# Kernel tuning notes

Hardware: AMD Instinct MI355X
Metric: run time of the kernel (lower is better)

Reference implementation:

```python
import jax, jax.numpy as jnp
import numpy as np

DIM = 256
NEG_SLOPE = 0.01  # torch F.leaky_relu default


def setup_inputs() -> dict:
    key = jax.random.key(0)
    ks = jax.random.split(key, 10)
    B, O, I, D = 16, 64, 512, DIM
    q = jax.random.normal(ks[0], (B, O, D), dtype=jnp.float32)
    k = jax.random.normal(ks[1], (B, I, D), dtype=jnp.float32)
    v = jax.random.normal(ks[2], (B, I, D), dtype=jnp.float32)
    mask = jax.random.randint(ks[3], (B, I), 0, 2).astype(bool)  # 1/True = pad
    s = 1.0 / np.sqrt(2 * D)
    # score MLP: Linear(2D -> D), tanh, Linear(D -> 1)
    W1 = jax.random.normal(ks[4], (D, 2 * D), dtype=jnp.float32) * s
    b1 = jnp.zeros((D,), dtype=jnp.float32)
    W2 = jax.random.normal(ks[5], (1, D), dtype=jnp.float32) * (1.0 / np.sqrt(D))
    b2 = jnp.zeros((1,), dtype=jnp.float32)
    # output projection fw: Linear(D -> D)
    Wf = jax.random.normal(ks[6], (D, D), dtype=jnp.float32) * (1.0 / np.sqrt(D))
    bf = jnp.zeros((D,), dtype=jnp.float32)
    return {"q": q, "k": k, "v": v, "mask": mask,
            "W1": W1, "b1": b1, "W2": W2, "b2": b2, "Wf": Wf, "bf": bf}


def reference(q, k, v, mask, W1, b1, W2, b2, Wf, bf):
    # Linear over concat([q, k]) decomposes exactly: W1 @ [q;k] = W1q@q + W1k@k
    D = q.shape[-1]
    W1q, W1k = W1[:, :D], W1[:, D:]
    qp = jnp.einsum('bod,hd->boh', q, W1q)          # (B, O, D)
    kp = jnp.einsum('bid,hd->bih', k, W1k)          # (B, I, D)
    h = jnp.tanh(qp[:, :, None, :] + kp[:, None, :, :] + b1)  # (B, O, I, D)
    score = jnp.einsum('boih,h->boi', h, W2[0]) + b2[0]       # (B, O, I)
    score = jnp.where(mask[:, None, :], -jnp.inf, score)
    attn = jax.nn.softmax(score, axis=-1)           # (B, O, I)
    out = jnp.einsum('boi,bid->bod', attn, v)       # (B, O, D)
    out = out @ Wf.T + bf                           # dropout in eval mode = identity
    out = jnp.where(out >= 0, out, NEG_SLOPE * out) # leaky_relu
    return out, attn
```

## Files before the change

kernel.cpp:

```cpp
#include <hip/hip_runtime.h>
#include <math.h>

#define DIM 256
#define BATCH 16
#define NO 64
#define NI 512
#define NEG_SLOPE 0.01f
#define CSCALE 2.885390081777927f
#define OT 2

typedef float f32x4 __attribute__((ext_vector_type(4)));
typedef __bf16 bf16x8 __attribute__((ext_vector_type(8)));
typedef unsigned int u32x4 __attribute__((ext_vector_type(4)));

__global__ __launch_bounds__(512) void mask_scan_kernel(
    const int* __restrict__ mask, int* __restrict__ idx,
    int* __restrict__ posArr, int* __restrict__ cnt)
{
  __shared__ int wtot[8];
  __shared__ int woff[8];
  const int b = blockIdx.x, t = threadIdx.x;
  const int lane = t & 63, wid = t >> 6;
  const int unm = (mask[b * NI + t] == 0) ? 1 : 0;
  unsigned long long bal = __ballot(unm);
  int my  = __popcll(bal & ((1ull << lane) - 1ull));
  if (lane == 0) wtot[wid] = __popcll(bal);
  __syncthreads();
  if (t == 0) {
    int acc = 0;
    for (int w = 0; w < 8; ++w) { woff[w] = acc; acc += wtot[w]; }
    cnt[b] = acc;
  }
  __syncthreads();
  int pos = woff[wid] + my;
  if (unm) idx[b * NI + pos] = t;
  posArr[b * NI + t] = unm ? pos : -1;
}

__device__ __forceinline__ void split2(float f, unsigned int& hi16, float& lo) {
  unsigned int u = __builtin_bit_cast(unsigned int, f);
  unsigned int h = (u + 0x7FFFu + ((u >> 16) & 1u)) & 0xFFFF0000u;
  hi16 = h >> 16;
  lo = f - __builtin_bit_cast(float, h);
}
__device__ __forceinline__ unsigned int rne16(float f) {
  unsigned int u = __builtin_bit_cast(unsigned int, f);
  return (u + 0x7FFFu + ((u >> 16) & 1u)) >> 16;
}

struct __align__(8) U2 { unsigned int x, y; };

#define OFF_AH 0
#define OFF_AL 9216
#define OFF_WH 18432
#define OFF_WL 27648

__global__ __launch_bounds__(256, 4) void proj_kernel(
    const float* __restrict__ q, const float* __restrict__ k,
    const float* __restrict__ W1, const float* __restrict__ b1,
    const float* __restrict__ Wf, const int* __restrict__ posArr,
    float* __restrict__ Eq, float* __restrict__ Ek4, float* __restrict__ WfT)
{
  __shared__ __align__(16) char smemRaw[36864];

  const int t  = threadIdx.x;
  const int bx = blockIdx.x;

  if (bx >= 576) {
    float* smem = (float*)smemRaw;
    const int tt = bx - 576;
    const int tr = tt >> 2, tc = tt & 3;
#pragma unroll
    for (int p = 0; p < 4; ++p) {
      int idx2 = p * 256 + t;
      int row = idx2 >> 4, j = idx2 & 15;
      float4 vv = *(const float4*)(Wf + (size_t)(tr * 64 + row) * 256 + tc * 64 + j * 4);
      *(float4*)&smem[row * 68 + j * 4] = vv;
    }
    __syncthreads();
#pragma unroll
    for (int p = 0; p < 4; ++p) {
      int idx2 = p * 256 + t;
      int row = idx2 >> 4, j = idx2 & 15;
      float4 ov;
      ov.x = smem[(j * 4 + 0) * 68 + row];
      ov.y = smem[(j * 4 + 1) * 68 + row];
      ov.z = smem[(j * 4 + 2) * 68 + row];
      ov.w = smem[(j * 4 + 3) * 68 + row];
      *(float4*)(WfT + (size_t)(tc * 64 + row) * 256 + tr * 64 + j * 4) = ov;
    }
    return;
  }

  const int mt = bx >> 2;
  const int nt = bx & 3;
  const int r0 = mt * 64;
  const int h0 = nt * 64;
  const bool isq = (r0 < BATCH * NO);
  const float* src = isq ? (q + (size_t)r0 * DIM)
                         : (k + (size_t)(r0 - BATCH * NO) * DIM);
  const int coff = isq ? 0 : DIM;

  const int srow = t >> 4;
  const int sc4  = t & 15;

  const int lane = t & 63, w = t >> 6;
  const int m0w = (w >> 1) * 32, n0w = (w & 1) * 32;
  const int lr = lane & 15, lg = lane >> 4;

  f32x4 acc[2][2] = {};

  float4 aR[4], wR[4];
#define LOADC(c0_)                                                              \
  _Pragma("unroll")                                                             \
  for (int p = 0; p < 4; ++p) {                                                 \
    int row = srow + p * 16;                                                    \
    aR[p] = *(const float4*)(src + (size_t)row * DIM + (c0_) + sc4 * 4);        \
    wR[p] = *(const float4*)(W1 + (size_t)(h0 + row) * (2 * DIM) + coff + (c0_) + sc4 * 4); \
  }

  LOADC(0)

  for (int c = 0; c < 4; ++c) {
#pragma unroll
    for (int p = 0; p < 4; ++p) {
      int row = srow + p * 16;
      int boff = row * 144 + sc4 * 8;
      unsigned int h0_, h1_, h2_, h3_;
      float l0, l1, l2, l3;
      split2(aR[p].x, h0_, l0); split2(aR[p].y, h1_, l1);
      split2(aR[p].z, h2_, l2); split2(aR[p].w, h3_, l3);
      *(U2*)(smemRaw + OFF_AH + boff) = { h0_ | (h1_ << 16), h2_ | (h3_ << 16) };
      *(U2*)(smemRaw + OFF_AL + boff) = { rne16(l0) | (rne16(l1) << 16),
                                          rne16(l2) | (rne16(l3) << 16) };
      split2(wR[p].x, h0_, l0); split2(wR[p].y, h1_, l1);
      split2(wR[p].z, h2_, l2); split2(wR[p].w, h3_, l3);
      *(U2*)(smemRaw + OFF_WH + boff) = { h0_ | (h1_ << 16), h2_ | (h3_ << 16) };
      *(U2*)(smemRaw + OFF_WL + boff) = { rne16(l0) | (rne16(l1) << 16),
                                          rne16(l2) | (rne16(l3) << 16) };
    }
    __syncthreads();

    if (c < 3) { LOADC((c + 1) * 64) }

#pragma unroll
    for (int kk = 0; kk < 2; ++kk) {
      const int kb = kk * 64 + lg * 16;
      bf16x8 ah[2], al[2], bh[2], bl[2];
#pragma unroll
      for (int mi = 0; mi < 2; ++mi) {
        int row = m0w + mi * 16 + lr;
        ah[mi] = __builtin_bit_cast(bf16x8, *(const u32x4*)(smemRaw + OFF_AH + row * 144 + kb));
        al[mi] = __builtin_bit_cast(bf16x8, *(const u32x4*)(smemRaw + OFF_AL + row * 144 + kb));
      }
#pragma unroll
      for (int ni = 0; ni < 2; ++ni) {
        int row = n0w + ni * 16 + lr;
        bh[ni] = __builtin_bit_cast(bf16x8, *(const u32x4*)(smemRaw + OFF_WH + row * 144 + kb));
        bl[ni] = __builtin_bit_cast(bf16x8, *(const u32x4*)(smemRaw + OFF_WL + row * 144 + kb));
      }
#pragma unroll
      for (int mi = 0; mi < 2; ++mi)
#pragma unroll
        for (int ni = 0; ni < 2; ++ni) {
          acc[mi][ni] = __builtin_amdgcn_mfma_f32_16x16x32_bf16(ah[mi], bh[ni], acc[mi][ni], 0, 0, 0);
          acc[mi][ni] = __builtin_amdgcn_mfma_f32_16x16x32_bf16(ah[mi], bl[ni], acc[mi][ni], 0, 0, 0);
          acc[mi][ni] = __builtin_amdgcn_mfma_f32_16x16x32_bf16(al[mi], bh[ni], acc[mi][ni], 0, 0, 0);
        }
    }
    __syncthreads();
  }

  if (isq) {
#pragma unroll
    for (int ni = 0; ni < 2; ++ni) {
      int h = h0 + n0w + ni * 16 + lr;
      float b1v = b1[h];
#pragma unroll
      for (int mi = 0; mi < 2; ++mi)
#pragma unroll
        for (int rg = 0; rg < 4; ++rg) {
          int r = r0 + m0w + mi * 16 + lg * 4 + rg;
          Eq[(size_t)r * DIM + h] =
              __builtin_amdgcn_exp2f((acc[mi][ni][rg] + b1v) * CSCALE);
        }
    }
  } else {
    const int rk0 = r0 - BATCH * NO;
    const int b = rk0 >> 9;
    const int ib = rk0 & 511;
#pragma unroll
    for (int mi = 0; mi < 2; ++mi)
#pragma unroll
      for (int rg = 0; rg < 4; ++rg) {
        int i = ib + m0w + mi * 16 + lg * 4 + rg;
        int pos = posArr[b * NI + i];
        if (pos >= 0) {
#pragma unroll
          for (int ni = 0; ni < 2; ++ni) {
            int h = h0 + n0w + ni * 16 + lr;
            Ek4[((size_t)(b * 64 + (h >> 2)) * NI + pos) * 4 + (h & 3)] =
                __builtin_amdgcn_exp2f(acc[mi][ni][rg] * CSCALE);
          }
        }
      }
  }
}

__device__ __forceinline__ void f4arr(float4 v, float* a) {
  a[0] = v.x; a[1] = v.y; a[2] = v.z; a[3] = v.w;
}

__global__ __launch_bounds__(512, 4) void attn_kernel(
    const float* __restrict__ Eq, const float* __restrict__ Ek4,
    const float* __restrict__ v, const int* __restrict__ idx,
    const int* __restrict__ posArr, const int* __restrict__ cnt,
    const float* __restrict__ W2, const float* __restrict__ b2,
    const float* __restrict__ WfT, const float* __restrict__ bf,
    float* __restrict__ out, float* __restrict__ attn_out)
{
  __shared__ float sc[OT][NI];
  __shared__ int   idxs[NI];
  __shared__ float pvp[8][OT][DIM];
  __shared__ float o0[OT][DIM];
  __shared__ float red4[8][OT];
  __shared__ float redw[8];

  const int t    = threadIdx.x;
  const int lane = t & 63;
  const int wid  = t >> 6;

  const int blk  = blockIdx.x;
  const int tile = (blk & 7) * 64 + (blk >> 3);
  const int b    = tile >> 5;
  const int bo0  = b * 64 + (tile & 31) * OT;

  const int cntb = cnt[b];
  idxs[t] = idx[b * NI + t];
  const int myPos = posArr[b * NI + t];

  float partial = (t < DIM) ? W2[t] : 0.f;
#pragma unroll
  for (int off = 32; off >= 1; off >>= 1) partial += __shfl_xor(partial, off, 64);
  if (lane == 0) redw[wid] = partial;
  __syncthreads();
  float sumw2 = 0.f;
#pragma unroll
  for (int w = 0; w < 8; ++w) sumw2 += redw[w];
  const float base = sumw2 + b2[0];

  const int j = t;
  const bool active = (j < cntb);
  const int jc = active ? j : (cntb > 0 ? cntb - 1 : 0);
  const float4* kb4 = (const float4*)Ek4 + (size_t)b * 64 * NI;
  const float* qrow0 = Eq + (size_t)(bo0 + 0) * DIM;
  const float* qrow1 = Eq + (size_t)(bo0 + 1) * DIM;

  float acc0 = 0.f, acc1 = 0.f;
  if (wid * 64 < cntb) {
#pragma unroll 8
    for (int hq = 0; hq < 64; ++hq) {
      float4 kq = kb4[(size_t)hq * NI + jc];
      float wr[4], q0r[4], q1r[4], kv[4];
      f4arr(*(const float4*)(W2 + hq * 4), wr);
      f4arr(*(const float4*)(qrow0 + hq * 4), q0r);
      f4arr(*(const float4*)(qrow1 + hq * 4), q1r);
      f4arr(kq, kv);
#pragma unroll
      for (int pr = 0; pr < 2; ++pr) {
        const int ea = pr * 2, eb = pr * 2 + 1;
        float A0 = fmaf(q0r[ea], kv[ea], 1.f);
        float B0 = fmaf(q0r[eb], kv[eb], 1.f);
        float N0 = fmaf(wr[eb], A0, wr[ea] * B0);
        acc0 = fmaf(N0, __builtin_amdgcn_rcpf(A0 * B0), acc0);
        float A1 = fmaf(q1r[ea], kv[ea], 1.f);
        float B1 = fmaf(q1r[eb], kv[eb], 1.f);
        float N1 = fmaf(wr[eb], A1, wr[ea] * B1);
        acc1 = fmaf(N1, __builtin_amdgcn_rcpf(A1 * B1), acc1);
      }
    }
  }

  float s0 = active ? (base - 2.f * acc0) : -INFINITY;
  float s1 = active ? (base - 2.f * acc1) : -INFINITY;

  float p0 = __builtin_amdgcn_exp2f(s0 * 1.4426950408889634f);
  float p1 = __builtin_amdgcn_exp2f(s1 * 1.4426950408889634f);
  float ps0 = p0, ps1 = p1;
#pragma unroll
  for (int off = 32; off >= 1; off >>= 1) {
    ps0 += __shfl_xor(ps0, off, 64);
    ps1 += __shfl_xor(ps1, off, 64);
  }
  __syncthreads();
  if (lane == 0) { red4[wid][0] = ps0; red4[wid][1] = ps1; }
  __syncthreads();
  float ss0 = 0.f, ss1 = 0.f;
#pragma unroll
  for (int w = 0; w < 8; ++w) { ss0 += red4[w][0]; ss1 += red4[w][1]; }
  const float a0 = p0 * __builtin_amdgcn_rcpf(ss0);
  const float a1 = p1 * __builtin_amdgcn_rcpf(ss1);
  sc[0][j] = a0;
  sc[1][j] = a1;
  __syncthreads();

  {
    float w0 = (myPos >= 0) ? sc[0][myPos] : 0.f;
    float w1 = (myPos >= 0) ? sc[1][myPos] : 0.f;
    attn_out[(size_t)(bo0 + 0) * NI + t] = w0;
    attn_out[(size_t)(bo0 + 1) * NI + t] = w1;
  }

  {
    const int d4 = lane;
    float4 av0 = {0.f, 0.f, 0.f, 0.f};
    float4 av1 = {0.f, 0.f, 0.f, 0.f};
    const float4* vb4 = (const float4*)(v + (size_t)b * NI * DIM);
    const int jend = min(wid * 64 + 64, cntb);
#pragma unroll 4
    for (int jb = wid * 64; jb < jend; ++jb) {
      int row = idxs[jb];
      float sa0 = sc[0][jb], sa1 = sc[1][jb];
      float4 vv = vb4[(size_t)row * 64 + d4];
      av0.x = fmaf(sa0, vv.x, av0.x);
      av0.y = fmaf(sa0, vv.y, av0.y);
      av0.z = fmaf(sa0, vv.z, av0.z);
      av0.w = fmaf(sa0, vv.w, av0.w);
      av1.x = fmaf(sa1, vv.x, av1.x);
      av1.y = fmaf(sa1, vv.y, av1.y);
      av1.z = fmaf(sa1, vv.z, av1.z);
      av1.w = fmaf(sa1, vv.w, av1.w);
    }
    *(float4*)&pvp[wid][0][d4 * 4] = av0;
    *(float4*)&pvp[wid][1][d4 * 4] = av1;
  }
  __syncthreads();
  {
    int oo = t >> 8, d = t & 255;
    float sacc = 0.f;
#pragma unroll
    for (int w = 0; w < 8; ++w) sacc += pvp[w][oo][d];
    o0[oo][d] = sacc;
  }
  __syncthreads();

  if (t < DIM) {
    const int d = t;
    float f0 = 0.f, f1 = 0.f;
#pragma unroll 8
    for (int e4 = 0; e4 < 64; ++e4) {
      float oa[4], ob[4];
      f4arr(*(const float4*)&o0[0][e4 * 4], oa);
      f4arr(*(const float4*)&o0[1][e4 * 4], ob);
#pragma unroll
      for (int c = 0; c < 4; ++c) {
        float wv = WfT[(size_t)(e4 * 4 + c) * DIM + d];
        f0 = fmaf(oa[c], wv, f0);
        f1 = fmaf(ob[c], wv, f1);
      }
    }
    float bfv = bf[d];
    f0 += bfv; f1 += bfv;
    f0 = (f0 >= 0.f) ? f0 : NEG_SLOPE * f0;
    f1 = (f1 >= 0.f) ? f1 : NEG_SLOPE * f1;
    out[(size_t)(bo0 + 0) * DIM + d] = f0;
    out[(size_t)(bo0 + 1) * DIM + d] = f1;
  }
}

extern "C" void kernel_launch(void* const* d_in, const int* in_sizes, int n_in,
                              void* d_out, int out_size, void* d_ws, size_t ws_size,
                              hipStream_t stream) {
  const float* q    = (const float*)d_in[0];
  const float* k    = (const float*)d_in[1];
  const float* v    = (const float*)d_in[2];
  const int*   mask = (const int*)d_in[3];
  const float* W1   = (const float*)d_in[4];
  const float* b1   = (const float*)d_in[5];
  const float* W2   = (const float*)d_in[6];
  const float* b2   = (const float*)d_in[7];
  const float* Wf   = (const float*)d_in[8];
  const float* bf   = (const float*)d_in[9];

  float* out      = (float*)d_out;
  float* attn_out = out + (size_t)BATCH * NO * DIM;

  float* Eq   = (float*)d_ws;
  float* Ek4  = Eq + (size_t)BATCH * NO * DIM;
  float* WfT  = Ek4 + (size_t)BATCH * DIM * NI;
  int*   idx  = (int*)(WfT + (size_t)DIM * DIM);
  int*   pos  = idx + BATCH * NI;
  int*   cnt  = pos + BATCH * NI;

  mask_scan_kernel<<<BATCH, 512, 0, stream>>>(mask, idx, pos, cnt);
  proj_kernel<<<592, 256, 0, stream>>>(q, k, W1, b1, Wf, pos, Eq, Ek4, WfT);
  attn_kernel<<<(BATCH * NO) / OT, 512, 0, stream>>>(Eq, Ek4, v, idx, pos, cnt,
                                                     W2, b2, WfT, bf, out, attn_out);
}
```

Measured before the change: 124.2 us.

## Fuse mask scan into projection and attention kernels, project only unmasked keys

Removes the separate mask_scan kernel launch. Each key-projection block now recomputes the per-batch prefix scan over the mask, gathers only unmasked key rows into its tile, and exits early when the tile lies beyond the unmasked count. This skips projection work for padded keys, which is about half of them with the test mask. The attention kernel recomputes the compacted index and positions from the mask with ballots. The cost is redundant scans in every block and gathered row loads.

```diff
diff --git a/kernel.cpp b/kernel.cpp
--- a/kernel.cpp
+++ b/kernel.cpp
@@ -13,30 +13,6 @@
 typedef __bf16 bf16x8 __attribute__((ext_vector_type(8)));
 typedef unsigned int u32x4 __attribute__((ext_vector_type(4)));
 
-__global__ __launch_bounds__(512) void mask_scan_kernel(
-    const int* __restrict__ mask, int* __restrict__ idx,
-    int* __restrict__ posArr, int* __restrict__ cnt)
-{
-  __shared__ int wtot[8];
-  __shared__ int woff[8];
-  const int b = blockIdx.x, t = threadIdx.x;
-  const int lane = t & 63, wid = t >> 6;
-  const int unm = (mask[b * NI + t] == 0) ? 1 : 0;
-  unsigned long long bal = __ballot(unm);
-  int my  = __popcll(bal & ((1ull << lane) - 1ull));
-  if (lane == 0) wtot[wid] = __popcll(bal);
-  __syncthreads();
-  if (t == 0) {
-    int acc = 0;
-    for (int w = 0; w < 8; ++w) { woff[w] = acc; acc += wtot[w]; }
-    cnt[b] = acc;
-  }
-  __syncthreads();
-  int pos = woff[wid] + my;
-  if (unm) idx[b * NI + pos] = t;
-  posArr[b * NI + t] = unm ? pos : -1;
-}
-
 __device__ __forceinline__ void split2(float f, unsigned int& hi16, float& lo) {
   unsigned int u = __builtin_bit_cast(unsigned int, f);
   unsigned int h = (u + 0x7FFFu + ((u >> 16) & 1u)) & 0xFFFF0000u;
@@ -58,10 +34,12 @@
 __global__ __launch_bounds__(256, 4) void proj_kernel(
     const float* __restrict__ q, const float* __restrict__ k,
     const float* __restrict__ W1, const float* __restrict__ b1,
-    const float* __restrict__ Wf, const int* __restrict__ posArr,
+    const float* __restrict__ Wf, const int* __restrict__ mask,
     float* __restrict__ Eq, float* __restrict__ Ek4, float* __restrict__ WfT)
 {
   __shared__ __align__(16) char smemRaw[36864];
+  __shared__ int idx_s[64];
+  __shared__ int swtot[4];
 
   const int t  = threadIdx.x;
   const int bx = blockIdx.x;
@@ -94,19 +72,58 @@
 
   const int mt = bx >> 2;
   const int nt = bx & 3;
-  const int r0 = mt * 64;
   const int h0 = nt * 64;
-  const bool isq = (r0 < BATCH * NO);
-  const float* src = isq ? (q + (size_t)r0 * DIM)
-                         : (k + (size_t)(r0 - BATCH * NO) * DIM);
-  const int coff = isq ? 0 : DIM;
+  const bool isq = (mt < 16);
 
   const int srow = t >> 4;
   const int sc4  = t & 15;
-
   const int lane = t & 63, w = t >> 6;
   const int m0w = (w >> 1) * 32, n0w = (w & 1) * 32;
   const int lr = lane & 15, lg = lane >> 4;
+
+  const float* src;
+  int coff, bb = 0, jb0 = 0, cntb = 0;
+  int rowg[4];
+
+  if (isq) {
+    src  = q + (size_t)(mt * 64) * DIM;
+    coff = 0;
+#pragma unroll
+    for (int p = 0; p < 4; ++p) rowg[p] = srow + p * 16;
+  } else {
+    const int ki = mt - 16;
+    bb  = ki >> 3;
+    jb0 = (ki & 7) * 64;
+    const int e0 = (mask[bb * NI + 2 * t] == 0);
+    const int e1 = (mask[bb * NI + 2 * t + 1] == 0);
+    const int ps = e0 + e1;
+    int x = ps;
+#pragma unroll
+    for (int off = 1; off < 64; off <<= 1) {
+      int y = __shfl_up(x, off, 64);
+      if (lane >= off) x += y;
+    }
+    if (lane == 63) swtot[w] = x;
+    if (t < 64) idx_s[t] = 0;
+    __syncthreads();
+    int woffv = 0;
+#pragma unroll
+    for (int w2 = 0; w2 < 4; ++w2) {
+      int v_ = swtot[w2];
+      if (w2 < w) woffv += v_;
+      cntb += v_;
+    }
+    const int excl = woffv + x - ps;
+    const int p0 = excl, p1 = excl + e0;
+    if (e0 && p0 >= jb0 && p0 < jb0 + 64) idx_s[p0 - jb0] = 2 * t;
+    if (e1 && p1 >= jb0 && p1 < jb0 + 64) idx_s[p1 - jb0] = 2 * t + 1;
+    __syncthreads();
+    if (jb0 >= cntb) return;
+    src  = k + (size_t)bb * NI * DIM;
+    coff = DIM;
+#pragma unroll
+    for (int p = 0; p < 4; ++p) rowg[p] = idx_s[srow + p * 16];
+  }
 
   f32x4 acc[2][2] = {};
 
@@ -114,9 +131,8 @@
 #define LOADC(c0_)                                                              \
   _Pragma("unroll")                                                             \
   for (int p = 0; p < 4; ++p) {                                                 \
-    int row = srow + p * 16;                                                    \
-    aR[p] = *(const float4*)(src + (size_t)row * DIM + (c0_) + sc4 * 4);        \
-    wR[p] = *(const float4*)(W1 + (size_t)(h0 + row) * (2 * DIM) + coff + (c0_) + sc4 * 4); \
+    aR[p] = *(const float4*)(src + (size_t)rowg[p] * DIM + (c0_) + sc4 * 4);    \
+    wR[p] = *(const float4*)(W1 + (size_t)(h0 + srow + p * 16) * (2 * DIM) + coff + (c0_) + sc4 * 4); \
   }
 
   LOADC(0)
@@ -172,6 +188,7 @@
   }
 
   if (isq) {
+    const int r0 = mt * 64;
 #pragma unroll
     for (int ni = 0; ni < 2; ++ni) {
       int h = h0 + n0w + ni * 16 + lr;
@@ -186,20 +203,18 @@
         }
     }
   } else {
-    const int rk0 = r0 - BATCH * NO;
-    const int b = rk0 >> 9;
-    const int ib = rk0 & 511;
+    const int lim = cntb - jb0;
 #pragma unroll
     for (int mi = 0; mi < 2; ++mi)
 #pragma unroll
       for (int rg = 0; rg < 4; ++rg) {
-        int i = ib + m0w + mi * 16 + lg * 4 + rg;
-        int pos = posArr[b * NI + i];
-        if (pos >= 0) {
+        int local = m0w + mi * 16 + lg * 4 + rg;
+        if (local < lim) {
+          int pos = jb0 + local;
 #pragma unroll
           for (int ni = 0; ni < 2; ++ni) {
             int h = h0 + n0w + ni * 16 + lr;
-            Ek4[((size_t)(b * 64 + (h >> 2)) * NI + pos) * 4 + (h & 3)] =
+            Ek4[((size_t)(bb * 64 + (h >> 2)) * NI + pos) * 4 + (h & 3)] =
                 __builtin_amdgcn_exp2f(acc[mi][ni][rg] * CSCALE);
           }
         }
@@ -213,8 +228,7 @@
 
 __global__ __launch_bounds__(512, 4) void attn_kernel(
     const float* __restrict__ Eq, const float* __restrict__ Ek4,
-    const float* __restrict__ v, const int* __restrict__ idx,
-    const int* __restrict__ posArr, const int* __restrict__ cnt,
+    const float* __restrict__ v, const int* __restrict__ mask,
     const float* __restrict__ W2, const float* __restrict__ b2,
     const float* __restrict__ WfT, const float* __restrict__ bf,
     float* __restrict__ out, float* __restrict__ attn_out)
@@ -225,6 +239,7 @@
   __shared__ float o0[OT][DIM];
   __shared__ float red4[8][OT];
   __shared__ float redw[8];
+  __shared__ int   swtot8[8];
 
   const int t    = threadIdx.x;
   const int lane = t & 63;
@@ -235,15 +250,27 @@
   const int b    = tile >> 5;
   const int bo0  = b * 64 + (tile & 31) * OT;
 
-  const int cntb = cnt[b];
-  idxs[t] = idx[b * NI + t];
-  const int myPos = posArr[b * NI + t];
+  const int unm = (mask[b * NI + t] == 0) ? 1 : 0;
+  unsigned long long bal = __ballot(unm);
+  int my = __popcll(bal & ((1ull << lane) - 1ull));
+  if (lane == 0) swtot8[wid] = __popcll(bal);
 
   float partial = (t < DIM) ? W2[t] : 0.f;
 #pragma unroll
   for (int off = 32; off >= 1; off >>= 1) partial += __shfl_xor(partial, off, 64);
   if (lane == 0) redw[wid] = partial;
   __syncthreads();
+
+  int cntb = 0, woffv = 0;
+#pragma unroll
+  for (int w = 0; w < 8; ++w) {
+    int v_ = swtot8[w];
+    if (w < wid) woffv += v_;
+    cntb += v_;
+  }
+  const int myPos = unm ? (woffv + my) : -1;
+  if (unm) idxs[myPos] = t;
+
   float sumw2 = 0.f;
 #pragma unroll
   for (int w = 0; w < 8; ++w) sumw2 += redw[w];
@@ -388,12 +415,8 @@
   float* Eq   = (float*)d_ws;
   float* Ek4  = Eq + (size_t)BATCH * NO * DIM;
   float* WfT  = Ek4 + (size_t)BATCH * DIM * NI;
-  int*   idx  = (int*)(WfT + (size_t)DIM * DIM);
-  int*   pos  = idx + BATCH * NI;
-  int*   cnt  = pos + BATCH * NI;
-
-  mask_scan_kernel<<<BATCH, 512, 0, stream>>>(mask, idx, pos, cnt);
-  proj_kernel<<<592, 256, 0, stream>>>(q, k, W1, b1, Wf, pos, Eq, Ek4, WfT);
-  attn_kernel<<<(BATCH * NO) / OT, 512, 0, stream>>>(Eq, Ek4, v, idx, pos, cnt,
+
+  proj_kernel<<<592, 256, 0, stream>>>(q, k, W1, b1, Wf, mask, Eq, Ek4, WfT);
+  attn_kernel<<<(BATCH * NO) / OT, 512, 0, stream>>>(Eq, Ek4, v, mask,
                                                      W2, b2, WfT, bf, out, attn_out);
 }
```

Measured after the change: 121.6 us. -2.0%, faster.
